# Kernel optimization log

Hardware: AMD Instinct MI355X
Metric: run time of the kernel (lower is better)

Reference implementation:

```python
import jax, jax.numpy as jnp
import numpy as np

SEQ, BS, H, D = 2048, 2, 16, 64


def phi(x):
    # ELU(x / d**0.25) + 1
    return jax.nn.elu(x / (x.shape[-1] ** 0.25)) + 1.0


def setup_inputs() -> dict:
    key = jax.random.key(0)
    ks = jax.random.split(key, 5)
    return {
        "query_layer": jax.random.normal(ks[0], (SEQ, BS, H, D), jnp.float32),
        "key_layer": jax.random.normal(ks[1], (SEQ, BS, H, D), jnp.float32),
        "value_layer": jax.random.normal(ks[2], (SEQ, BS, H, D), jnp.float32),
        "attention_mask": jnp.zeros((BS, 1, SEQ, SEQ), dtype=bool),  # unused by forward
        "phi_k": jax.random.normal(ks[3], (1, H, D, 1), jnp.float32) / 10000.0,
        "phi_kv": jax.random.normal(ks[4], (1, H, D, D), jnp.float32) / 10000.0,
    }


def _ntk_attn(q, k, v, sum_phi_k, sum_phi_kv):
    # q,k,v: [bs,h,n,d]; sum_phi_k: [1,h,d,1]; sum_phi_kv: [1,h,d,d]
    d = q.shape[-1]
    nq, nk = q.shape[-2], k.shape[-2]
    kk = jnp.abs(sum_phi_k)
    Z = sum_phi_kv
    phi_q = phi(q)  # [bs,h,nq,d]
    A = jnp.einsum("bhqd,bhkd->bhqk", q, k) / jnp.sqrt(jnp.float32(d))
    max_A = jnp.max(A, axis=-1, keepdims=True)  # [bs,h,nq,1]
    exp_max_A = jnp.exp(max_A)
    A = jnp.exp(A - max_A)
    causal = jnp.tril(jnp.ones((nq, nk), jnp.float32), k=nk - nq)
    A = A * causal  # broadcast over [bs,h]
    D_norm = jnp.sum(A, axis=-1, keepdims=True) + jnp.matmul(phi_q, kk) / exp_max_A
    ctx = (jnp.matmul(A, v) + jnp.matmul(phi_q, Z) / exp_max_A) / D_norm
    return ctx  # [bs,h,nq,d]


def reference(query_layer, key_layer, value_layer, attention_mask, phi_k, phi_kv):
    # inputs are [seq, bs, h, d]; attention_mask is unused (module ignores it)
    q = jnp.transpose(query_layer, (1, 2, 0, 3)).astype(jnp.float32)
    k = jnp.transpose(key_layer, (1, 2, 0, 3)).astype(jnp.float32)
    v = jnp.transpose(value_layer, (1, 2, 0, 3)).astype(jnp.float32)
    ctx = _ntk_attn(q, k, v, phi_k, phi_kv)  # [bs,h,nq,d]
    ctx = jnp.transpose(ctx, (2, 0, 1, 3))  # [nq,bs,h,d]
    nq, bs, h, d = ctx.shape
    return ctx.reshape(nq, bs, h * d).astype(query_layer.dtype)
```

## Files before the change

kernel.cpp:

```cpp
#include <hip/hip_runtime.h>

#define SEQ 2048
#define BSZ 2
#define NHEAD 16
#define NBH (BSZ * NHEAD)
#define HDIM 64
#define QBLK 128
#define KVBLK 64
#define NQT (SEQ / QBLK)
#define ROWSTRIDE (BSZ * NHEAD * HDIM)

typedef __bf16 bf16x8 __attribute__((ext_vector_type(8)));
typedef __bf16 bf16x4 __attribute__((ext_vector_type(4)));
typedef float f32x4 __attribute__((ext_vector_type(4)));

#define AS1 __attribute__((address_space(1)))
#define AS3 __attribute__((address_space(3)))

__global__ __launch_bounds__(256)
void conv_all(const float* __restrict__ Kg, const float* __restrict__ Vg,
              const float* __restrict__ PKVg, __bf16* __restrict__ Kb,
              __bf16* __restrict__ Vt, __bf16* __restrict__ Ztb) {
  __shared__ __bf16 tt[HDIM][72];
  const int b = blockIdx.x;
  const int tid = threadIdx.x;

  if (b < 2048) {
    const int t = b * 256 + tid;
    const int s = t >> 8;
    const int bh = (t >> 3) & 31;
    const int d8 = (t & 7) * 8;
    const float* src = Kg + (size_t)s * ROWSTRIDE + bh * HDIM + d8;
    const float4 a = *(const float4*)src;
    const float4 bb = *(const float4*)(src + 4);
    bf16x8 o = {(__bf16)a.x, (__bf16)a.y, (__bf16)a.z, (__bf16)a.w,
                (__bf16)bb.x, (__bf16)bb.y, (__bf16)bb.z, (__bf16)bb.w};
    const int slot = (d8 >> 3) ^ (s & 7);
    *(bf16x8*)(Kb + ((size_t)bh * SEQ + s) * HDIM + slot * 8) = o;
  } else if (b < 3072) {
    const int t = b - 2048;
    const int kb = t & 31, bh = t >> 5;
    {
      const int r = tid >> 2, c16 = (tid & 3) * 16;
#pragma unroll
      for (int i = 0; i < 4; ++i) {
        const float4 v = *(const float4*)(Vg + (size_t)(kb * 64 + r) * ROWSTRIDE +
                                          bh * HDIM + c16 + 4 * i);
        tt[c16 + 4 * i + 0][r] = (__bf16)v.x;
        tt[c16 + 4 * i + 1][r] = (__bf16)v.y;
        tt[c16 + 4 * i + 2][r] = (__bf16)v.z;
        tt[c16 + 4 * i + 3][r] = (__bf16)v.w;
      }
    }
    __syncthreads();
    {
      const int d = tid >> 2, c2 = (tid & 3) * 2;
#pragma unroll
      for (int k8 = 0; k8 < 2; ++k8) {
        const int s8 = c2 + k8;
        const int pbase = (s8 ^ (d & 7)) * 8;
        __bf16 ov[8];
#pragma unroll
        for (int j = 0; j < 8; ++j) {
          const int p = pbase + j;
          const int P = p >> 5, g = (p >> 3) & 3, jj = p & 7;
          ov[j] = tt[d][32 * P + 16 * (jj >> 2) + 4 * g + (jj & 3)];
        }
        *(bf16x8*)(Vt + (((size_t)bh * 32 + kb) * 64 + d) * 64 + s8 * 8) =
            *(const bf16x8*)ov;
      }
    }
  } else {
    const int t = (b - 3072) * 256 + tid;
    const int lr = t & 15, lg = (t >> 4) & 3, c = (t >> 6) & 1;
    const int dj = (t >> 7) & 3, h = t >> 9;
    __bf16 o[8];
#pragma unroll
    for (int i = 0; i < 8; ++i)
      o[i] = (__bf16)PKVg[((size_t)h * 64 + 32 * c + 8 * lg + i) * 64 + dj * 16 + lr];
    *(bf16x8*)(Ztb + (size_t)t * 8) = *(const bf16x8*)o;
  }
}

__global__ __launch_bounds__(256, 2)
void ntk_attn(const float* __restrict__ Qg, const __bf16* __restrict__ Kb,
              const __bf16* __restrict__ Vt, const float* __restrict__ PKg,
              const __bf16* __restrict__ Ztb, float* __restrict__ Og) {
  __shared__ __bf16 Ks[2][KVBLK * HDIM];
  __shared__ __bf16 Vts[2][KVBLK * HDIM];

  const int tid = threadIdx.x;
  const int w = tid >> 6, l = tid & 63, lr = l & 15, lg = l >> 4;

  const int ord = blockIdx.x;
  const int bh = ord & 31, h = bh & (NHEAD - 1);
  const int v = ord >> 5;
  const int bx = (v < 8) ? v : 23 - v;
  const int q0 = bx * QBLK;
  const int ntile = 2 * bx + 2;
  const int dt0 = 2 * bx;
  const int headoff = bh * HDIM;
  const __bf16* Kbh = Kb + (size_t)bh * SEQ * HDIM;
  const __bf16* Vbh = Vt + (size_t)bh * SEQ * HDIM;

  auto stage = [&](int kb, int bb) {
    const char* gk = (const char*)Kbh + ((size_t)kb << 13) + (w << 11) + (l << 4);
    const char* gv = (const char*)Vbh + ((size_t)kb << 13) + (w << 11) + (l << 4);
    __bf16* lk = &Ks[bb][w << 10];
    __bf16* lv = &Vts[bb][w << 10];
    __builtin_amdgcn_global_load_lds((const AS1 unsigned*)gk,
                                     (AS3 unsigned*)lk, 16, 0, 0);
    __builtin_amdgcn_global_load_lds((const AS1 unsigned*)(gk + 1024),
                                     (AS3 unsigned*)(lk + 512), 16, 0, 0);
    __builtin_amdgcn_global_load_lds((const AS1 unsigned*)gv,
                                     (AS3 unsigned*)lv, 16, 0, 0);
    __builtin_amdgcn_global_load_lds((const AS1 unsigned*)(gv + 1024),
                                     (AS3 unsigned*)(lv + 512), 16, 0, 0);
  };

  stage(0, 0);

  bf16x8 aq[2][2], pq[2][2];
#pragma unroll
  for (int g = 0; g < 2; ++g) {
    const float* qp = Qg + (size_t)(q0 + 64 * g + w * 16 + lr) * ROWSTRIDE +
                      headoff + lg * 8;
#pragma unroll
    for (int c = 0; c < 2; ++c) {
      const float4 x0 = *(const float4*)(qp + 32 * c);
      const float4 x1 = *(const float4*)(qp + 32 * c + 4);
      const float f[8] = {x0.x, x0.y, x0.z, x0.w, x1.x, x1.y, x1.z, x1.w};
#pragma unroll
      for (int i = 0; i < 8; ++i) {
        aq[g][c][i] = (__bf16)(f[i] * 0.18033688011112042f);
        const float xs = f[i] * 0.3535533905932738f;
        pq[g][c][i] = (__bf16)(xs > 0.f ? xs + 1.f : __expf(xs));
      }
    }
  }

  const f32x4 z4 = {0.f, 0.f, 0.f, 0.f};
  f32x4 oacc[2][4] = {{z4, z4, z4, z4}, {z4, z4, z4, z4}};
  float lsum[2] = {0.f, 0.f};
  int qa[2];
  qa[0] = q0 + w * 16 + lr;
  qa[1] = q0 + 64 + w * 16 + lr;
  const int sw = lr & 7;

  __syncthreads();
  int cur = 0;

  for (int kb = 0; kb < ntile; ++kb) {
    const bool more = (kb + 1 < ntile);
    if (more) stage(kb + 1, cur ^ 1);

    bf16x8 kc[4][2];
#pragma unroll
    for (int nj = 0; nj < 4; ++nj)
#pragma unroll
      for (int c = 0; c < 2; ++c)
        kc[nj][c] = *(const bf16x8*)&Ks[cur][(nj * 16 + lr) * 64 +
                                            (((4 * c + lg) ^ sw) << 3)];
    bf16x8 vv[2][4];
#pragma unroll
    for (int P = 0; P < 2; ++P)
#pragma unroll
      for (int dj = 0; dj < 4; ++dj)
        vv[P][dj] = *(const bf16x8*)&Vts[cur][(dj * 16 + lr) * 64 +
                                             (((4 * P + lg) ^ sw) << 3)];

    const int kv0 = kb * KVBLK;
#pragma unroll
    for (int g = 0; g < 2; ++g) {
      if (g == 0 && kb > dt0) continue;

      f32x4 s4[4];
      __builtin_amdgcn_s_setprio(1);
#pragma unroll
      for (int nj = 0; nj < 4; ++nj) {
        f32x4 acc = z4;
        acc = __builtin_amdgcn_mfma_f32_16x16x32_bf16(kc[nj][0], aq[g][0], acc, 0, 0, 0);
        acc = __builtin_amdgcn_mfma_f32_16x16x32_bf16(kc[nj][1], aq[g][1], acc, 0, 0, 0);
        s4[nj] = acc;
      }
      __builtin_amdgcn_s_setprio(0);

      bf16x4 p4[4];
      const bool diag = (kb == dt0 + g);
#pragma unroll
      for (int nj = 0; nj < 4; ++nj) {
#pragma unroll
        for (int r = 0; r < 4; ++r) {
          float e;
          if (diag) {
            const int kabs = kv0 + 16 * nj + 4 * lg + r;
            e = (kabs <= qa[g]) ? __builtin_amdgcn_exp2f(s4[nj][r]) : 0.f;
          } else {
            e = __builtin_amdgcn_exp2f(s4[nj][r]);
          }
          lsum[g] += e;
          p4[nj][r] = (__bf16)e;
        }
      }

      __builtin_amdgcn_s_setprio(1);
#pragma unroll
      for (int P = 0; P < 2; ++P) {
        const bf16x8 pa = __builtin_shufflevector(p4[2 * P], p4[2 * P + 1],
                                                  0, 1, 2, 3, 4, 5, 6, 7);
#pragma unroll
        for (int dj = 0; dj < 4; ++dj)
          oacc[g][dj] = __builtin_amdgcn_mfma_f32_16x16x32_bf16(pa, vv[P][dj],
                                                                oacc[g][dj], 0, 0, 0);
      }
      __builtin_amdgcn_s_setprio(0);
    }

    if (more) {
      __syncthreads();
      cur ^= 1;
    }
  }

  float ka[16];
  {
#pragma unroll
    for (int c = 0; c < 2; ++c) {
      const float* kp = PKg + h * HDIM + 32 * c + 8 * lg;
      const float4 a = *(const float4*)kp;
      const float4 b = *(const float4*)(kp + 4);
      ka[8 * c + 0] = fabsf(a.x); ka[8 * c + 1] = fabsf(a.y);
      ka[8 * c + 2] = fabsf(a.z); ka[8 * c + 3] = fabsf(a.w);
      ka[8 * c + 4] = fabsf(b.x); ka[8 * c + 5] = fabsf(b.y);
      ka[8 * c + 6] = fabsf(b.z); ka[8 * c + 7] = fabsf(b.w);
    }
  }
  bf16x8 bz[2][4];
  const __bf16* Zf = Ztb + (size_t)h * 4096;
#pragma unroll
  for (int c = 0; c < 2; ++c)
#pragma unroll
    for (int dj = 0; dj < 4; ++dj)
      bz[c][dj] = *(const bf16x8*)(Zf + ((dj * 2 + c) * 64 + l) * 8);

#pragma unroll
  for (int g = 0; g < 2; ++g) {
    float pkk = 0.f;
#pragma unroll
    for (int c = 0; c < 2; ++c)
#pragma unroll
      for (int i = 0; i < 8; ++i)
        pkk += (float)pq[g][c][i] * ka[8 * c + i];
    pkk += __shfl_xor(pkk, 16);
    pkk += __shfl_xor(pkk, 32);
    float s = lsum[g];
    s += __shfl_xor(s, 16);
    s += __shfl_xor(s, 32);
    const float den = s + pkk;

    f32x4 zacc[4] = {z4, z4, z4, z4};
    __builtin_amdgcn_s_setprio(1);
#pragma unroll
    for (int c = 0; c < 2; ++c)
#pragma unroll
      for (int dj = 0; dj < 4; ++dj)
        zacc[dj] = __builtin_amdgcn_mfma_f32_16x16x32_bf16(pq[g][c], bz[c][dj],
                                                           zacc[dj], 0, 0, 0);
    __builtin_amdgcn_s_setprio(0);

#pragma unroll
    for (int r = 0; r < 4; ++r) {
      const float rd = 1.f / __shfl(den, lg * 4 + r);
      float* op = Og + (size_t)(q0 + 64 * g + w * 16 + lg * 4 + r) * ROWSTRIDE +
                  headoff;
#pragma unroll
      for (int dj = 0; dj < 4; ++dj)
        op[dj * 16 + lr] = (oacc[g][dj][r] + zacc[dj][r]) * rd;
    }
  }
}

extern "C" void kernel_launch(void* const* d_in, const int* in_sizes, int n_in,
                              void* d_out, int out_size, void* d_ws, size_t ws_size,
                              hipStream_t stream) {
  const float* Qg  = (const float*)d_in[0];
  const float* Kg  = (const float*)d_in[1];
  const float* Vg  = (const float*)d_in[2];
  const float* PKg  = (const float*)d_in[4];
  const float* PKVg = (const float*)d_in[5];
  float* Og = (float*)d_out;

  __bf16* Kb  = (__bf16*)d_ws;
  __bf16* Vt  = Kb + (size_t)NBH * SEQ * HDIM;
  __bf16* Ztb = Vt + (size_t)NBH * SEQ * HDIM;

  conv_all<<<dim3(2048 + 1024 + 32), dim3(256), 0, stream>>>(Kg, Vg, PKVg,
                                                             Kb, Vt, Ztb);
  ntk_attn<<<dim3(NQT * NBH), dim3(256), 0, stream>>>(Qg, Kb, Vt, PKg, Ztb, Og);
}
```

Baseline: 46.48 us.

## Halve query block to 64 rows with 2-wave blocks and more CTAs

```diff
diff --git a/kernel.cpp b/kernel.cpp
--- a/kernel.cpp
+++ b/kernel.cpp
@@ -5,7 +5,7 @@
 #define NHEAD 16
 #define NBH (BSZ * NHEAD)
 #define HDIM 64
-#define QBLK 128
+#define QBLK 64
 #define KVBLK 64
 #define NQT (SEQ / QBLK)
 #define ROWSTRIDE (BSZ * NHEAD * HDIM)
@@ -82,7 +82,7 @@
   }
 }
 
-__global__ __launch_bounds__(256, 2)
+__global__ __launch_bounds__(128, 2)
 void ntk_attn(const float* __restrict__ Qg, const __bf16* __restrict__ Kb,
               const __bf16* __restrict__ Vt, const float* __restrict__ PKg,
               const __bf16* __restrict__ Ztb, float* __restrict__ Og) {
@@ -95,36 +95,36 @@
   const int ord = blockIdx.x;
   const int bh = ord & 31, h = bh & (NHEAD - 1);
   const int v = ord >> 5;
-  const int bx = (v < 8) ? v : 23 - v;
+  const int bx = (v < 16) ? v : 47 - v;
   const int q0 = bx * QBLK;
-  const int ntile = 2 * bx + 2;
-  const int dt0 = 2 * bx;
+  const int ntile = bx + 1;
   const int headoff = bh * HDIM;
   const __bf16* Kbh = Kb + (size_t)bh * SEQ * HDIM;
   const __bf16* Vbh = Vt + (size_t)bh * SEQ * HDIM;
 
   auto stage = [&](int kb, int bb) {
-    const char* gk = (const char*)Kbh + ((size_t)kb << 13) + (w << 11) + (l << 4);
-    const char* gv = (const char*)Vbh + ((size_t)kb << 13) + (w << 11) + (l << 4);
-    __bf16* lk = &Ks[bb][w << 10];
-    __bf16* lv = &Vts[bb][w << 10];
-    __builtin_amdgcn_global_load_lds((const AS1 unsigned*)gk,
-                                     (AS3 unsigned*)lk, 16, 0, 0);
-    __builtin_amdgcn_global_load_lds((const AS1 unsigned*)(gk + 1024),
-                                     (AS3 unsigned*)(lk + 512), 16, 0, 0);
-    __builtin_amdgcn_global_load_lds((const AS1 unsigned*)gv,
-                                     (AS3 unsigned*)lv, 16, 0, 0);
-    __builtin_amdgcn_global_load_lds((const AS1 unsigned*)(gv + 1024),
-                                     (AS3 unsigned*)(lv + 512), 16, 0, 0);
+    const char* gk = (const char*)Kbh + ((size_t)kb << 13) + (w << 12) + (l << 4);
+    const char* gv = (const char*)Vbh + ((size_t)kb << 13) + (w << 12) + (l << 4);
+    __bf16* lk = &Ks[bb][w << 11];
+    __bf16* lv = &Vts[bb][w << 11];
+#pragma unroll
+    for (int i = 0; i < 4; ++i) {
+      __builtin_amdgcn_global_load_lds((const AS1 unsigned*)(gk + (i << 10)),
+                                       (AS3 unsigned*)(lk + (i << 9)), 16, 0, 0);
+      __builtin_amdgcn_global_load_lds((const AS1 unsigned*)(gv + (i << 10)),
+                                       (AS3 unsigned*)(lv + (i << 9)), 16, 0, 0);
+    }
   };
 
   stage(0, 0);
 
   bf16x8 aq[2][2], pq[2][2];
+  int qa[2];
 #pragma unroll
   for (int g = 0; g < 2; ++g) {
-    const float* qp = Qg + (size_t)(q0 + 64 * g + w * 16 + lr) * ROWSTRIDE +
-                      headoff + lg * 8;
+    const int qrow = q0 + (2 * g + w) * 16 + lr;
+    qa[g] = qrow;
+    const float* qp = Qg + (size_t)qrow * ROWSTRIDE + headoff + lg * 8;
 #pragma unroll
     for (int c = 0; c < 2; ++c) {
       const float4 x0 = *(const float4*)(qp + 32 * c);
@@ -141,10 +141,7 @@
 
   const f32x4 z4 = {0.f, 0.f, 0.f, 0.f};
   f32x4 oacc[2][4] = {{z4, z4, z4, z4}, {z4, z4, z4, z4}};
-  float lsum[2] = {0.f, 0.f};
-  int qa[2];
-  qa[0] = q0 + w * 16 + lr;
-  qa[1] = q0 + 64 + w * 16 + lr;
+  float ls[2][2] = {{0.f, 0.f}, {0.f, 0.f}};
   const int sw = lr & 7;
 
   __syncthreads();
@@ -169,13 +166,11 @@
         vv[P][dj] = *(const bf16x8*)&Vts[cur][(dj * 16 + lr) * 64 +
                                              (((4 * P + lg) ^ sw) << 3)];
 
+    const bool diag = (kb == bx);
     const int kv0 = kb * KVBLK;
 #pragma unroll
     for (int g = 0; g < 2; ++g) {
-      if (g == 0 && kb > dt0) continue;
-
       f32x4 s4[4];
-      __builtin_amdgcn_s_setprio(1);
 #pragma unroll
       for (int nj = 0; nj < 4; ++nj) {
         f32x4 acc = z4;
@@ -183,10 +178,8 @@
         acc = __builtin_amdgcn_mfma_f32_16x16x32_bf16(kc[nj][1], aq[g][1], acc, 0, 0, 0);
         s4[nj] = acc;
       }
-      __builtin_amdgcn_s_setprio(0);
 
       bf16x4 p4[4];
-      const bool diag = (kb == dt0 + g);
 #pragma unroll
       for (int nj = 0; nj < 4; ++nj) {
 #pragma unroll
@@ -198,12 +191,11 @@
           } else {
             e = __builtin_amdgcn_exp2f(s4[nj][r]);
           }
-          lsum[g] += e;
+          ls[g][nj & 1] += e;
           p4[nj][r] = (__bf16)e;
         }
       }
 
-      __builtin_amdgcn_s_setprio(1);
 #pragma unroll
       for (int P = 0; P < 2; ++P) {
         const bf16x8 pa = __builtin_shufflevector(p4[2 * P], p4[2 * P + 1],
@@ -213,7 +205,6 @@
           oacc[g][dj] = __builtin_amdgcn_mfma_f32_16x16x32_bf16(pa, vv[P][dj],
                                                                 oacc[g][dj], 0, 0, 0);
       }
-      __builtin_amdgcn_s_setprio(0);
     }
 
     if (more) {
@@ -223,17 +214,15 @@
   }
 
   float ka[16];
-  {
-#pragma unroll
-    for (int c = 0; c < 2; ++c) {
-      const float* kp = PKg + h * HDIM + 32 * c + 8 * lg;
-      const float4 a = *(const float4*)kp;
-      const float4 b = *(const float4*)(kp + 4);
-      ka[8 * c + 0] = fabsf(a.x); ka[8 * c + 1] = fabsf(a.y);
-      ka[8 * c + 2] = fabsf(a.z); ka[8 * c + 3] = fabsf(a.w);
-      ka[8 * c + 4] = fabsf(b.x); ka[8 * c + 5] = fabsf(b.y);
-      ka[8 * c + 6] = fabsf(b.z); ka[8 * c + 7] = fabsf(b.w);
-    }
+#pragma unroll
+  for (int c = 0; c < 2; ++c) {
+    const float* kp = PKg + h * HDIM + 32 * c + 8 * lg;
+    const float4 a = *(const float4*)kp;
+    const float4 b = *(const float4*)(kp + 4);
+    ka[8 * c + 0] = fabsf(a.x); ka[8 * c + 1] = fabsf(a.y);
+    ka[8 * c + 2] = fabsf(a.z); ka[8 * c + 3] = fabsf(a.w);
+    ka[8 * c + 4] = fabsf(b.x); ka[8 * c + 5] = fabsf(b.y);
+    ka[8 * c + 6] = fabsf(b.z); ka[8 * c + 7] = fabsf(b.w);
   }
   bf16x8 bz[2][4];
   const __bf16* Zf = Ztb + (size_t)h * 4096;
@@ -253,25 +242,23 @@
         pkk += (float)pq[g][c][i] * ka[8 * c + i];
     pkk += __shfl_xor(pkk, 16);
     pkk += __shfl_xor(pkk, 32);
-    float s = lsum[g];
+    float s = ls[g][0] + ls[g][1];
     s += __shfl_xor(s, 16);
     s += __shfl_xor(s, 32);
     const float den = s + pkk;
 
     f32x4 zacc[4] = {z4, z4, z4, z4};
-    __builtin_amdgcn_s_setprio(1);
 #pragma unroll
     for (int c = 0; c < 2; ++c)
 #pragma unroll
       for (int dj = 0; dj < 4; ++dj)
         zacc[dj] = __builtin_amdgcn_mfma_f32_16x16x32_bf16(pq[g][c], bz[c][dj],
                                                            zacc[dj], 0, 0, 0);
-    __builtin_amdgcn_s_setprio(0);
 
 #pragma unroll
     for (int r = 0; r < 4; ++r) {
       const float rd = 1.f / __shfl(den, lg * 4 + r);
-      float* op = Og + (size_t)(q0 + 64 * g + w * 16 + lg * 4 + r) * ROWSTRIDE +
+      float* op = Og + (size_t)(q0 + (2 * g + w) * 16 + lg * 4 + r) * ROWSTRIDE +
                   headoff;
 #pragma unroll
       for (int dj = 0; dj < 4; ++dj)
@@ -296,5 +283,5 @@
 
   conv_all<<<dim3(2048 + 1024 + 32), dim3(256), 0, stream>>>(Kg, Vg, PKVg,
                                                              Kb, Vt, Ztb);
-  ntk_attn<<<dim3(NQT * NBH), dim3(256), 0, stream>>>(Qg, Kb, Vt, PKg, Ztb, Og);
+  ntk_attn<<<dim3(NQT * NBH), dim3(128), 0, stream>>>(Qg, Kb, Vt, PKg, Ztb, Og);
 }
```

New measurement: 50.40 us. 8.4% more time.
